# Kernel optimization log

Hardware: AMD Instinct MI355X
Metric: run time of the kernel (lower is better)

Reference implementation:

```python
import jax, jax.numpy as jnp
import numpy as np

D = (96, 96, 96)          # per-item tensor shape (input_shape)
BATCH = 8
R1, R2 = 32, 16           # ranks for the two multi-resolution partitions
MAX_ITER = 15             # fixed ALS iteration count (torch default 100 w/ early stop)


def setup_inputs() -> dict:
    key = jax.random.key(0)
    k = jax.random.split(key, 5)
    m, n = D[0], D[1] * D[2]  # unfold: (first mode, rest) -> (96, 9216)
    return {
        "x": jax.random.normal(k[0], (BATCH,) + D, dtype=jnp.float32),
        "A0_1": jax.random.normal(k[1], (m, R1), dtype=jnp.float32),
        "B0_1": jax.random.normal(k[2], (n, R1), dtype=jnp.float32),
        "A0_2": jax.random.normal(k[3], (m, R2), dtype=jnp.float32),
        "B0_2": jax.random.normal(k[4], (n, R2), dtype=jnp.float32),
    }


def _clean(f):
    # torch.nan_to_num(f, nan=0.0, posinf=1e10, neginf=-1e10)
    return jnp.nan_to_num(f, nan=0.0, posinf=1e10, neginf=-1e10)


def _als(X, A, B):
    """2-mode PARAFAC == ALS matrix factorization. X: (m,n), A: (m,r), B: (n,r)."""
    def step(carry, _):
        A, B = carry
        # mode 0: khatri-rao prod is just B; V = B^T B; A = (X B) pinv(V)
        A = _clean((X @ B) @ jnp.linalg.pinv(B.T @ B))
        # mode 1: unfold is X^T; V = A^T A; B = (X^T A) pinv(V)
        B = _clean((X.T @ A) @ jnp.linalg.pinv(A.T @ A))
        return (A, B), None
    (A, B), _ = jax.lax.scan(step, (A, B), None, length=MAX_ITER)
    return A, B


def _per_item(t, A0_1, B0_1, A0_2, B0_2):
    m = D[0]
    # partition 1 ([[0],[1,2]]): unfold -> (96, 9216)
    X1 = t.reshape(m, -1)
    A1, B1 = _als(X1, A0_1, B0_1)
    approx1 = (A1 @ B1.T).reshape(D)
    residual = t - approx1
    # partition 2 ([[0,1],[2]]): same identity mode order -> same unfold shape
    X2 = residual.reshape(m, -1)
    A2, B2 = _als(X2, A0_2, B0_2)
    approx2 = (A2 @ B2.T).reshape(D)
    # reconstruct() = sum of partition approximations
    return approx1 + approx2


def reference(x, A0_1, B0_1, A0_2, B0_2):
    # per-item MRLR reconstruction, vmapped over the batch (torch loops per item)
    return jax.vmap(_per_item, in_axes=(0, None, None, None, None))(
        x, A0_1, B0_1, A0_2, B0_2
    )
```

## Files before the change

### kernel.cpp

```cpp
#include <hip/hip_runtime.h>


#define TID ((int)threadIdx.x)
typedef float4 f4;

#define SC27 (1.0f/134217728.0f)

__device__ __forceinline__ f4 ld4(const float* p) { return *(const f4*)p; }
__device__ __forceinline__ void st4(float* p, f4 v) { *(f4*)p = v; }
__device__ __forceinline__ f4 f4zero() { return make_float4(0.f,0.f,0.f,0.f); }
__device__ __forceinline__ f4 add4(f4 a, f4 b){ return make_float4(a.x+b.x,a.y+b.y,a.z+b.z,a.w+b.w); }
__device__ __forceinline__ f4 sub4(f4 a, f4 b){ return make_float4(a.x-b.x,a.y-b.y,a.z-b.z,a.w-b.w); }
__device__ __forceinline__ f4 scl4(f4 a, float s){ return make_float4(a.x*s,a.y*s,a.z*s,a.w*s); }
__device__ __forceinline__ void fma4(f4& a, float s, f4 v) {
  a.x = fmaf(s,v.x,a.x); a.y = fmaf(s,v.y,a.y); a.z = fmaf(s,v.z,a.z); a.w = fmaf(s,v.w,a.w);
}
__device__ __forceinline__ float dot4(f4 a, f4 b, float acc) {
  acc = fmaf(a.x,b.x,acc); acc = fmaf(a.y,b.y,acc);
  acc = fmaf(a.z,b.z,acc); acc = fmaf(a.w,b.w,acc); return acc;
}
__device__ __forceinline__ void trimap(int t, int& ti, int& tj) {
  int rem = t; ti = 0;
  #pragma unroll
  for (int r = 0; r < 12; ++r) { int w = 12 - r; if (rem < w) { ti = r; break; } rem -= w; }
  tj = ti + rem;
}
__device__ __forceinline__ void init8(f4 acc[8][2]) {
  #pragma unroll
  for (int a = 0; a < 8; ++a) { acc[a][0] = f4zero(); acc[a][1] = f4zero(); }
}
__device__ __forceinline__ void tile8_step(f4 acc[8][2], const float* u, const float* v) {
  f4 u0 = ld4(u), u1 = ld4(u+4), v0 = ld4(v), v1 = ld4(v+4);
  float aa[8] = {u0.x,u0.y,u0.z,u0.w,u1.x,u1.y,u1.z,u1.w};
  #pragma unroll
  for (int a = 0; a < 8; ++a) { fma4(acc[a][0], aa[a], v0); fma4(acc[a][1], aa[a], v1); }
}

__global__ __launch_bounds__(512) void k1_partials(
    const float* __restrict__ x, const float* __restrict__ b01,
    const float* __restrict__ b02, float* __restrict__ part,
    int nch, int nsc) {
  __shared__ __align__(16) float Xst[48][100];
  __shared__ __align__(16) float Bs[48][52];
  __shared__ __align__(16) float red[9600];
  int bid = blockIdx.x;
  int item = bid & 7, kc = bid >> 3;
  const float* X = x + (size_t)item * 96 * 9216;
  float* base = part + (size_t)(item * nch + kc) * 9600;

  int t = TID, kh = 0, tt = 0;
  const float* ap = nullptr; const float* bp = nullptr;
  float* op = nullptr; int os = 0; bool isM = false;
  bool active = (t < 450);
  if (active) {
    kh = t / 150; tt = t % 150;
    if (tt < 78) {
      int ti, tj; trimap(tt, ti, tj);
      ap = &Xst[0][ti*8]; bp = &Xst[0][tj*8];
      op = base + tt*64; os = 8; isM = true;
    } else {
      int u = tt - 78; int i0 = (u/6)*8, c0 = (u%6)*8;
      ap = &Xst[0][i0]; bp = &Bs[0][c0];
      op = base + 4992 + i0*48 + c0; os = 48;
    }
  }

  f4 acc[8][2]; init8(acc);

  for (int sc = 0; sc < nsc; ++sc) {
    int k0 = (kc * nsc + sc) * 48;
    __syncthreads();
    for (int e = TID; e < 1152; e += 512) {
      int i = e / 12, kq = (e % 12) * 4;
      f4 v = ld4(&X[(size_t)i * 9216 + k0 + kq]);
      Xst[kq][i] = v.x; Xst[kq+1][i] = v.y; Xst[kq+2][i] = v.z; Xst[kq+3][i] = v.w;
    }
    for (int e = TID; e < 384; e += 512) {
      int kk = e / 8, cq = (e % 8) * 4;
      st4(&Bs[kk][cq], ld4(&b01[(size_t)(k0 + kk) * 32 + cq]));
    }
    for (int e = TID; e < 192; e += 512) {
      int kk = e / 4, cq = (e % 4) * 4;
      st4(&Bs[kk][32+cq], ld4(&b02[(size_t)(k0 + kk) * 16 + cq]));
    }
    __syncthreads();
    if (active) {
      int asr = 100, bsr = isM ? 100 : 52;
      const float* ar = ap + kh * asr;
      const float* br = bp + kh * bsr;
      #pragma unroll 4
      for (int kk = kh; kk < 48; kk += 3) {
        tile8_step(acc, ar, br);
        ar += 3 * asr; br += 3 * bsr;
      }
    }
  }
  __syncthreads();
  if (active && kh == 1) {
    #pragma unroll
    for (int a = 0; a < 8; ++a) { st4(&red[tt*64+a*8], acc[a][0]); st4(&red[tt*64+a*8+4], acc[a][1]); }
  }
  __syncthreads();
  if (active && kh == 0) {
    #pragma unroll
    for (int a = 0; a < 8; ++a) {
      acc[a][0] = add4(acc[a][0], ld4(&red[tt*64+a*8]));
      acc[a][1] = add4(acc[a][1], ld4(&red[tt*64+a*8+4]));
    }
  }
  __syncthreads();
  if (active && kh == 2) {
    #pragma unroll
    for (int a = 0; a < 8; ++a) { st4(&red[tt*64+a*8], acc[a][0]); st4(&red[tt*64+a*8+4], acc[a][1]); }
  }
  __syncthreads();
  if (active && kh == 0) {
    #pragma unroll
    for (int a = 0; a < 8; ++a) {
      f4 s0 = add4(acc[a][0], ld4(&red[tt*64+a*8]));
      f4 s1 = add4(acc[a][1], ld4(&red[tt*64+a*8+4]));
      st4(op + a*os, s0); st4(op + a*os + 4, s1);
    }
  }
}

__global__ __launch_bounds__(128) void k2_reduce(
    const float* __restrict__ part, float* __restrict__ Mb,
    float* __restrict__ Cb, int nch) {
  int bid = blockIdx.x;
  int item = bid & 7, chunk = bid >> 3;
  if (TID >= 120) return;
  int q4 = chunk * 120 + TID;
  int off = q4 * 4;
  const float* p = part + (size_t)item * nch * 9600 + off;
  f4 s = f4zero();
  #pragma unroll 8
  for (int c = 0; c < nch; ++c) s = add4(s, ld4(p + (size_t)c * 9600));
  if (off < 4992) {
    int tile = off >> 6, w = (off & 63) >> 2;
    int r = w >> 1, cq = (w & 1) * 4;
    int ti, tj; trimap(tile, ti, tj);
    int i = ti*8 + r, j = tj*8 + cq;
    float* Mi = Mb + (size_t)item * 9216;
    st4(&Mi[i*96 + j], s);
    Mi[(j+0)*96 + i] = s.x; Mi[(j+1)*96 + i] = s.y;
    Mi[(j+2)*96 + i] = s.z; Mi[(j+3)*96 + i] = s.w;
  } else {
    st4(&Cb[(size_t)item * 4608 + (off - 4992)], s);
  }
}

__global__ __launch_bounds__(256) void kw_phase(
    const float* __restrict__ Ag, const float* __restrict__ Bg,
    const float* __restrict__ Subg, float* __restrict__ Dg, float scale,
    const float* __restrict__ Tin, int ti_istr, int tis, int tsub,
    float* __restrict__ Tout, int to_istr, int tos, int TW) {
  __shared__ __align__(16) float Bs[96][100];
  __shared__ __align__(16) float As[8][100];
  __shared__ __align__(16) float Ts[96][36];
  int bid = blockIdx.x;
  int item = bid & 7, w = bid >> 3, t = TID;
  const float* A = Ag + (size_t)item * 9216;

  if (w < 12) {
    const float* B = Bg + (size_t)item * 9216;
    for (int e = t; e < 2304; e += 256) {
      int r = e / 24, cq = (e % 24) * 4;
      st4(&Bs[r][cq], ld4(&B[r*96 + cq]));
    }
    if (t < 192) {
      int r = t / 24, cq = (t % 24) * 4;
      st4(&As[r][cq], ld4(&A[(size_t)(w*8 + r)*96 + cq]));
    }
    __syncthreads();
    if (t < 192) {
      int rl = t / 24, jb = (t % 24) * 4;
      f4 acc = f4zero();
      #pragma unroll 8
      for (int k = 0; k < 96; ++k) fma4(acc, As[rl][k], ld4(&Bs[k][jb]));
      int r = w*8 + rl;
      if (Subg) acc = sub4(ld4(&Subg[(size_t)item*9216 + r*96 + jb]), acc);
      else      acc = scl4(acc, scale);
      st4(&Dg[(size_t)item*9216 + r*96 + jb], acc);
    }
  } else {
    for (int e = t; e < 2304; e += 256) {
      int r = e / 24, cq = (e % 24) * 4;
      st4(&Bs[r][cq], ld4(&A[r*96 + cq]));
    }
    int nq = TW >> 2;
    const float* Ti = Tin + (size_t)item * ti_istr;
    for (int e = t; e < 96*nq; e += 256) {
      int r = e / nq, cq = (e % nq) * 4;
      st4(&Ts[r][cq], ld4(&Ti[(size_t)r * tis + cq]));
    }
    __syncthreads();
    int nact = (TW == 32) ? 192 : 96;
    if (t < nact) {
      int r  = (TW == 32) ? (t >> 1) : t;
      int c0 = (TW == 32) ? (t & 1) * 16 : 0;
      f4 acc[4] = {f4zero(), f4zero(), f4zero(), f4zero()};
      #pragma unroll 4
      for (int k = 0; k < 96; ++k) {
        float a = Bs[r][k];
        const float* tr = &Ts[k][c0];
        fma4(acc[0], a, ld4(tr));   fma4(acc[1], a, ld4(tr+4));
        fma4(acc[2], a, ld4(tr+8)); fma4(acc[3], a, ld4(tr+12));
      }
      if (tsub) {
        #pragma unroll
        for (int u = 0; u < 4; ++u) acc[u] = sub4(ld4(&Ts[r][c0 + u*4]), acc[u]);
      }
      float* To = Tout + (size_t)item * to_istr;
      #pragma unroll
      for (int u = 0; u < 4; ++u) st4(&To[(size_t)r * tos + c0 + u*4], acc[u]);
    }
  }
}

template<int R>
__device__ void gj_wave(float (*aug)[64], int lane) {
  float col[R];
  if (lane < R) {
    #pragma unroll
    for (int i = 0; i < R; ++i) col[i] = aug[i][lane];
  } else {
    #pragma unroll
    for (int i = 0; i < R; ++i) col[i] = (i == lane - R) ? 1.f : 0.f;
  }
  #pragma unroll
  for (int c = 0; c < R; ++c) {
    float pc = __shfl(col[c], c);
    float rp = 1.f / pc;
    bool isc = (lane == c);
    #pragma unroll
    for (int i = 0; i < R; ++i) {
      if (i == c) continue;
      float fi = __shfl(col[i], c) * rp;
      float v = fmaf(-fi, col[c], col[i]);
      col[i] = isc ? 0.f : v;
    }
  }
  #pragma unroll
  for (int i = 0; i < R; ++i) {
    float d = __shfl(col[i], i);
    col[i] = col[i] / d;
  }
  if (lane >= R) {
    #pragma unroll
    for (int i = 0; i < R; ++i) aug[i][lane] = col[i];
  }
}

template<int TW, int MODE>
__global__ __launch_bounds__(256) void kWproj(
    const float* __restrict__ S3g, const float* __restrict__ Pg,
    float* __restrict__ W1g, float* __restrict__ Tgg) {
  __shared__ __align__(16) float S3s[96][100];
  __shared__ __align__(16) float Ps[96][32];
  __shared__ __align__(16) float Qs[96][32];
  __shared__ __align__(16) float aug[32][64];
  __shared__ __align__(16) float QKs[8][32];

  int bid = blockIdx.x;
  int item = bid & 7, w = bid >> 3, t = TID;
  const float* S3 = S3g + (size_t)item * 9216;
  const float* P  = Pg  + (size_t)item * 3072;
  float* W1 = W1g + (size_t)item * 9216;
  float* Tg = Tgg + (size_t)item * 9216;
  const int nq = TW >> 2;

  for (int e = t; e < 2304; e += 256) {
    int r = e / 24, cq = (e % 24) * 4;
    st4(&S3s[r][cq], ld4(&S3[r*96 + cq]));
  }
  for (int e = t; e < 96*nq; e += 256) {
    int r = e / nq, cq = (e % nq) * 4;
    st4(&Ps[r][cq], ld4(&P[r*32 + cq]));
  }
  __syncthreads();

  for (int e = t; e < 96*nq; e += 256) {
    int r = e / nq, c4 = (e % nq) * 4;
    f4 acc = f4zero();
    #pragma unroll 4
    for (int k = 0; k < 96; ++k) fma4(acc, S3s[r][k], ld4(&Ps[k][c4]));
    st4(&Qs[r][c4], acc);
  }
  __syncthreads();

  for (int e = t; e < TW*nq; e += 256) {
    int ar = e / nq, b4 = (e % nq) * 4;
    f4 acc = f4zero();
    #pragma unroll 4
    for (int k = 0; k < 96; ++k) fma4(acc, Qs[k][ar], ld4(&Qs[k][b4]));
    st4(&aug[ar][b4], acc);
  }
  __syncthreads();

  if (t < 2*TW) gj_wave<TW>(aug, t);
  __syncthreads();
  for (int e = t; e < TW*TW; e += 256) { int m = e/TW, c = e%TW; aug[c][m] = aug[m][TW+c]; }
  __syncthreads();

  for (int e = t; e < 8*TW; e += 256) {
    int rr = e / TW, c = e % TW;
    const float* qrow = &Qs[w*8 + rr][0];
    float acc = 0.f;
    #pragma unroll
    for (int m4 = 0; m4 < TW; m4 += 4)
      acc = dot4(ld4(&qrow[m4]), ld4(&aug[c][m4]), acc);
    QKs[rr][c] = acc;
  }
  __syncthreads();

  if (t < 192) {
    int rr = t / 24, jb = (t % 24) * 4;
    int r = w*8 + rr;
    f4 acc = f4zero();
    #pragma unroll
    for (int c4 = 0; c4 < TW; c4 += 4) {
      f4 qk = ld4(&QKs[rr][c4]);
      acc.x = dot4(qk, ld4(&Qs[jb+0][c4]), acc.x);
      acc.y = dot4(qk, ld4(&Qs[jb+1][c4]), acc.y);
      acc.z = dot4(qk, ld4(&Qs[jb+2][c4]), acc.z);
      acc.w = dot4(qk, ld4(&Qs[jb+3][c4]), acc.w);
    }
    if (MODE == 1) st4(&W1[r*96 + jb], acc);
    else           st4(&Tg[r*96 + jb], add4(acc, ld4(&W1[r*96 + jb])));
  }
}

__global__ __launch_bounds__(256) void k4_out(
    const float* __restrict__ x, const float* __restrict__ Tgg,
    float* __restrict__ out) {
  __shared__ __align__(16) float Tt[96][100];
  int bid = blockIdx.x;
  int item = bid & 7, jb = bid >> 3;
  const float* Tg = Tgg + (size_t)item * 9216;
  for (int e = TID * 4; e < 9216; e += 1024) {
    f4 v = ld4(&Tg[e]);
    int i = e / 96, k = e % 96;
    Tt[k][i] = v.x; Tt[k+1][i] = v.y; Tt[k+2][i] = v.z; Tt[k+3][i] = v.w;
  }
  __syncthreads();

  int jq = (TID % 32) * 4, ig = TID / 32;
  int i0 = ig * 12;
  int col = jb * 128 + jq;
  const float* X = x + (size_t)item * 96 * 9216;
  f4 acc[12];
  #pragma unroll
  for (int a = 0; a < 12; ++a) acc[a] = f4zero();

  for (int k = 0; k < 96; ++k) {
    f4 xv = ld4(&X[(size_t)k * 9216 + col]);
    f4 t0 = ld4(&Tt[k][i0]), t1 = ld4(&Tt[k][i0+4]), t2 = ld4(&Tt[k][i0+8]);
    fma4(acc[0], t0.x, xv); fma4(acc[1], t0.y, xv); fma4(acc[2], t0.z, xv); fma4(acc[3], t0.w, xv);
    fma4(acc[4], t1.x, xv); fma4(acc[5], t1.y, xv); fma4(acc[6], t1.z, xv); fma4(acc[7], t1.w, xv);
    fma4(acc[8], t2.x, xv); fma4(acc[9], t2.y, xv); fma4(acc[10], t2.z, xv); fma4(acc[11], t2.w, xv);
  }
  float* O = out + (size_t)item * 96 * 9216;
  #pragma unroll
  for (int a = 0; a < 12; ++a) st4(&O[(size_t)(i0 + a) * 9216 + col], acc[a]);
}

extern "C" void kernel_launch(void* const* d_in, const int* in_sizes, int n_in,
                              void* d_out, int out_size, void* d_ws, size_t ws_size,
                              hipStream_t stream) {
  (void)in_sizes; (void)n_in; (void)out_size;
  const float* x   = (const float*)d_in[0];
  const float* b01 = (const float*)d_in[2];
  const float* b02 = (const float*)d_in[4];
  float* out = (float*)d_out;
  float* ws  = (float*)d_ws;

  const size_t EXTRA = 73728ull*6 + 36864 + 24576*2 + 12288;
  int nch = (ws_size >= ((size_t)64*8*9600 + EXTRA) * sizeof(float)) ? 64 : 32;
  int nsc = 9216 / nch / 48;

  float* Mb  = ws + (size_t)nch * 8 * 9600;
  float* Cb  = Mb  + 73728;
  float* Sb  = Cb  + 36864;
  float* S2b = Sb  + 73728;
  float* S3b = S2b + 73728;
  float* W1b = S3b + 73728;
  float* Tgb = W1b + 73728;
  float* Pb  = Tgb + 73728;
  float* Yb  = Pb  + 24576;
  float* CPb = Yb  + 24576;

  k1_partials<<<dim3(nch*8), 512, 0, stream>>>(x, b01, b02, ws, nch, nsc);
  k2_reduce<<<dim3(160), 128, 0, stream>>>(ws, Mb, Cb, nch);

  kw_phase<<<dim3(96),256,0,stream>>>(Mb, Mb, nullptr, Sb, SC27,
      nullptr,0,0,0, nullptr,0,0, 0);
  kw_phase<<<dim3(104),256,0,stream>>>(Sb, Sb, nullptr, S2b, 1.f,
      Cb,4608,48,0, Yb,3072,32, 32);
  kw_phase<<<dim3(104),256,0,stream>>>(S2b, S2b, nullptr, S3b, 1.f,
      Yb,3072,32,0, Pb,3072,32, 32);
  kWproj<32,1><<<dim3(96),256,0,stream>>>(S3b, Pb, W1b, Tgb);

  kw_phase<<<dim3(104),256,0,stream>>>(W1b, Mb, Mb, Sb, 1.f,
      Cb+32,4608,48,1, CPb,1536,16, 16);
  kw_phase<<<dim3(96),256,0,stream>>>(Sb, W1b, Sb, Mb, 1.f,
      nullptr,0,0,0, nullptr,0,0, 0);

  kw_phase<<<dim3(96),256,0,stream>>>(Mb, Mb, nullptr, Sb, SC27,
      nullptr,0,0,0, nullptr,0,0, 0);
  kw_phase<<<dim3(104),256,0,stream>>>(Sb, Sb, nullptr, S2b, 1.f,
      CPb,1536,16,0, Yb,3072,32, 16);
  kw_phase<<<dim3(104),256,0,stream>>>(S2b, S2b, nullptr, S3b, 1.f,
      Yb,3072,32,0, Pb,3072,32, 16);
  kWproj<16,2><<<dim3(96),256,0,stream>>>(S3b, Pb, W1b, Tgb);

  k4_out<<<dim3(576), 256, 0, stream>>>(x, Tgb, out);
}
```

Measured before the change: 181.4 us.

## Fuse reduce and small-matrix phases into one persistent kernel with grid barriers

Replaces the k2_reduce launch and the chain of kw_phase and kWproj launches with one cooperative kernel of 104 workgroups. The workgroups synchronise through an atomic grid barrier held in workspace and zeroed by a memset before each run. This removes about a dozen kernel launch gaps on a small latency-bound workload. The S3 product is also restructured into thin slab products (S2·(S2·Y)), so the full 96x96 S3 matrix is no longer formed. The change relies on all 104 workgroups being resident at the same time, and the spin barrier could deadlock if they are not.

```diff
diff --git a/kernel.cpp b/kernel.cpp
--- a/kernel.cpp
+++ b/kernel.cpp
@@ -5,6 +5,7 @@
 typedef float4 f4;
 
 #define SC27 (1.0f/134217728.0f)
+#define NWG  104
 
 __device__ __forceinline__ f4 ld4(const float* p) { return *(const f4*)p; }
 __device__ __forceinline__ void st4(float* p, f4 v) { *(f4*)p = v; }
@@ -34,6 +35,24 @@
   float aa[8] = {u0.x,u0.y,u0.z,u0.w,u1.x,u1.y,u1.z,u1.w};
   #pragma unroll
   for (int a = 0; a < 8; ++a) { fma4(acc[a][0], aa[a], v0); fma4(acc[a][1], aa[a], v1); }
+}
+
+__device__ __forceinline__ void gridbar(unsigned* bar, unsigned nwg) {
+  __syncthreads();
+  if (threadIdx.x == 0) {
+    __threadfence();
+    unsigned g = __hip_atomic_load(bar + 1, __ATOMIC_RELAXED, __HIP_MEMORY_SCOPE_AGENT);
+    unsigned a = __hip_atomic_fetch_add(bar, 1u, __ATOMIC_ACQ_REL, __HIP_MEMORY_SCOPE_AGENT);
+    if (a == nwg - 1u) {
+      __hip_atomic_store(bar, 0u, __ATOMIC_RELAXED, __HIP_MEMORY_SCOPE_AGENT);
+      __hip_atomic_store(bar + 1, g + 1u, __ATOMIC_RELEASE, __HIP_MEMORY_SCOPE_AGENT);
+    } else {
+      while (__hip_atomic_load(bar + 1, __ATOMIC_ACQUIRE, __HIP_MEMORY_SCOPE_AGENT) == g)
+        __builtin_amdgcn_s_sleep(8);
+    }
+    __threadfence();
+  }
+  __syncthreads();
 }
 
 __global__ __launch_bounds__(512) void k1_partials(
@@ -124,106 +143,12 @@
   }
 }
 
-__global__ __launch_bounds__(128) void k2_reduce(
-    const float* __restrict__ part, float* __restrict__ Mb,
-    float* __restrict__ Cb, int nch) {
-  int bid = blockIdx.x;
-  int item = bid & 7, chunk = bid >> 3;
-  if (TID >= 120) return;
-  int q4 = chunk * 120 + TID;
-  int off = q4 * 4;
-  const float* p = part + (size_t)item * nch * 9600 + off;
-  f4 s = f4zero();
-  #pragma unroll 8
-  for (int c = 0; c < nch; ++c) s = add4(s, ld4(p + (size_t)c * 9600));
-  if (off < 4992) {
-    int tile = off >> 6, w = (off & 63) >> 2;
-    int r = w >> 1, cq = (w & 1) * 4;
-    int ti, tj; trimap(tile, ti, tj);
-    int i = ti*8 + r, j = tj*8 + cq;
-    float* Mi = Mb + (size_t)item * 9216;
-    st4(&Mi[i*96 + j], s);
-    Mi[(j+0)*96 + i] = s.x; Mi[(j+1)*96 + i] = s.y;
-    Mi[(j+2)*96 + i] = s.z; Mi[(j+3)*96 + i] = s.w;
-  } else {
-    st4(&Cb[(size_t)item * 4608 + (off - 4992)], s);
-  }
-}
-
-__global__ __launch_bounds__(256) void kw_phase(
-    const float* __restrict__ Ag, const float* __restrict__ Bg,
-    const float* __restrict__ Subg, float* __restrict__ Dg, float scale,
-    const float* __restrict__ Tin, int ti_istr, int tis, int tsub,
-    float* __restrict__ Tout, int to_istr, int tos, int TW) {
-  __shared__ __align__(16) float Bs[96][100];
-  __shared__ __align__(16) float As[8][100];
-  __shared__ __align__(16) float Ts[96][36];
-  int bid = blockIdx.x;
-  int item = bid & 7, w = bid >> 3, t = TID;
-  const float* A = Ag + (size_t)item * 9216;
-
-  if (w < 12) {
-    const float* B = Bg + (size_t)item * 9216;
-    for (int e = t; e < 2304; e += 256) {
-      int r = e / 24, cq = (e % 24) * 4;
-      st4(&Bs[r][cq], ld4(&B[r*96 + cq]));
-    }
-    if (t < 192) {
-      int r = t / 24, cq = (t % 24) * 4;
-      st4(&As[r][cq], ld4(&A[(size_t)(w*8 + r)*96 + cq]));
-    }
-    __syncthreads();
-    if (t < 192) {
-      int rl = t / 24, jb = (t % 24) * 4;
-      f4 acc = f4zero();
-      #pragma unroll 8
-      for (int k = 0; k < 96; ++k) fma4(acc, As[rl][k], ld4(&Bs[k][jb]));
-      int r = w*8 + rl;
-      if (Subg) acc = sub4(ld4(&Subg[(size_t)item*9216 + r*96 + jb]), acc);
-      else      acc = scl4(acc, scale);
-      st4(&Dg[(size_t)item*9216 + r*96 + jb], acc);
-    }
-  } else {
-    for (int e = t; e < 2304; e += 256) {
-      int r = e / 24, cq = (e % 24) * 4;
-      st4(&Bs[r][cq], ld4(&A[r*96 + cq]));
-    }
-    int nq = TW >> 2;
-    const float* Ti = Tin + (size_t)item * ti_istr;
-    for (int e = t; e < 96*nq; e += 256) {
-      int r = e / nq, cq = (e % nq) * 4;
-      st4(&Ts[r][cq], ld4(&Ti[(size_t)r * tis + cq]));
-    }
-    __syncthreads();
-    int nact = (TW == 32) ? 192 : 96;
-    if (t < nact) {
-      int r  = (TW == 32) ? (t >> 1) : t;
-      int c0 = (TW == 32) ? (t & 1) * 16 : 0;
-      f4 acc[4] = {f4zero(), f4zero(), f4zero(), f4zero()};
-      #pragma unroll 4
-      for (int k = 0; k < 96; ++k) {
-        float a = Bs[r][k];
-        const float* tr = &Ts[k][c0];
-        fma4(acc[0], a, ld4(tr));   fma4(acc[1], a, ld4(tr+4));
-        fma4(acc[2], a, ld4(tr+8)); fma4(acc[3], a, ld4(tr+12));
-      }
-      if (tsub) {
-        #pragma unroll
-        for (int u = 0; u < 4; ++u) acc[u] = sub4(ld4(&Ts[r][c0 + u*4]), acc[u]);
-      }
-      float* To = Tout + (size_t)item * to_istr;
-      #pragma unroll
-      for (int u = 0; u < 4; ++u) st4(&To[(size_t)r * tos + c0 + u*4], acc[u]);
-    }
-  }
-}
-
 template<int R>
-__device__ void gj_wave(float (*aug)[64], int lane) {
+__device__ void gj_wave(float* aug, int lane) {
   float col[R];
   if (lane < R) {
     #pragma unroll
-    for (int i = 0; i < R; ++i) col[i] = aug[i][lane];
+    for (int i = 0; i < R; ++i) col[i] = aug[i*68 + lane];
   } else {
     #pragma unroll
     for (int i = 0; i < R; ++i) col[i] = (i == lane - R) ? 1.f : 0.f;
@@ -248,86 +173,271 @@
   }
   if (lane >= R) {
     #pragma unroll
-    for (int i = 0; i < R; ++i) aug[i][lane] = col[i];
-  }
-}
-
-template<int TW, int MODE>
-__global__ __launch_bounds__(256) void kWproj(
-    const float* __restrict__ S3g, const float* __restrict__ Pg,
-    float* __restrict__ W1g, float* __restrict__ Tgg) {
-  __shared__ __align__(16) float S3s[96][100];
-  __shared__ __align__(16) float Ps[96][32];
-  __shared__ __align__(16) float Qs[96][32];
-  __shared__ __align__(16) float aug[32][64];
-  __shared__ __align__(16) float QKs[8][32];
-
-  int bid = blockIdx.x;
-  int item = bid & 7, w = bid >> 3, t = TID;
-  const float* S3 = S3g + (size_t)item * 9216;
-  const float* P  = Pg  + (size_t)item * 3072;
-  float* W1 = W1g + (size_t)item * 9216;
-  float* Tg = Tgg + (size_t)item * 9216;
-  const int nq = TW >> 2;
-
+    for (int i = 0; i < R; ++i) aug[i*68 + lane] = col[i];
+  }
+}
+
+__device__ __forceinline__ void stage_full(float* Bs, const float* src, int t) {
   for (int e = t; e < 2304; e += 256) {
     int r = e / 24, cq = (e % 24) * 4;
-    st4(&S3s[r][cq], ld4(&S3[r*96 + cq]));
-  }
+    st4(&Bs[r*100 + cq], ld4(&src[r*96 + cq]));
+  }
+}
+__device__ __forceinline__ void stage_slab(float* As, const float* src, int row0, int t) {
+  if (t < 192) {
+    int r = t / 24, cq = (t % 24) * 4;
+    st4(&As[r*100 + cq], ld4(&src[(size_t)(row0 + r)*96 + cq]));
+  }
+}
+__device__ __forceinline__ void stage_thin(float* Ts, const float* src, int istr, int nq, int t) {
   for (int e = t; e < 96*nq; e += 256) {
     int r = e / nq, cq = (e % nq) * 4;
-    st4(&Ps[r][cq], ld4(&P[r*32 + cq]));
-  }
-  __syncthreads();
-
+    st4(&Ts[r*36 + cq], ld4(&src[(size_t)r*istr + cq]));
+  }
+}
+__device__ __forceinline__ void square_slab(const float* As, const float* Bs,
+    const float* Sub, float* D, float scale, int w, int t) {
+  if (t < 192) {
+    int rl = t / 24, jb = (t % 24) * 4;
+    f4 acc = f4zero();
+    #pragma unroll 8
+    for (int k = 0; k < 96; ++k) fma4(acc, As[rl*100 + k], ld4(&Bs[k*100 + jb]));
+    int r = w*8 + rl;
+    if (Sub) acc = sub4(ld4(&Sub[r*96 + jb]), acc);
+    else     acc = scl4(acc, scale);
+    st4(&D[r*96 + jb], acc);
+  }
+}
+__device__ __forceinline__ void thin_full(const float* A100, const float* Ts,
+    float* To, int tos, int TW, int tsub, int t) {
+  int nact = (TW == 32) ? 192 : 96;
+  if (t < nact) {
+    int r  = (TW == 32) ? (t >> 1) : t;
+    int c0 = (TW == 32) ? (t & 1) * 16 : 0;
+    f4 acc[4] = {f4zero(), f4zero(), f4zero(), f4zero()};
+    #pragma unroll 4
+    for (int k = 0; k < 96; ++k) {
+      float a = A100[r*100 + k];
+      const float* tr = &Ts[k*36 + c0];
+      fma4(acc[0], a, ld4(tr));   fma4(acc[1], a, ld4(tr+4));
+      fma4(acc[2], a, ld4(tr+8)); fma4(acc[3], a, ld4(tr+12));
+    }
+    if (tsub) {
+      #pragma unroll
+      for (int u = 0; u < 4; ++u) acc[u] = sub4(ld4(&Ts[r*36 + c0 + u*4]), acc[u]);
+    }
+    #pragma unroll
+    for (int u = 0; u < 4; ++u) st4(&To[(size_t)r*tos + c0 + u*4], acc[u]);
+  }
+}
+__device__ __forceinline__ void thin_slab(const float* As, const float* Ts,
+    float* To, int w, int TW, int t) {
+  int nq = TW >> 2;
+  if (t < 8*nq) {
+    int rl = t / nq, c4 = (t % nq) * 4;
+    f4 acc = f4zero();
+    #pragma unroll 8
+    for (int k = 0; k < 96; ++k) fma4(acc, As[rl*100 + k], ld4(&Ts[k*36 + c4]));
+    st4(&To[(size_t)(w*8 + rl)*32 + c4], acc);
+  }
+}
+
+template<int TW>
+__device__ void proj_phase(const float* Bs , float* Ps, float* Qs,
+    float* aug, float* QKs, const float* Pg, float* Wdst, const float* Wadd,
+    int w, int t) {
+  const int nq = TW >> 2;
+  stage_thin(Ps, Pg, 32, nq, t);
+  __syncthreads();
   for (int e = t; e < 96*nq; e += 256) {
     int r = e / nq, c4 = (e % nq) * 4;
     f4 acc = f4zero();
     #pragma unroll 4
-    for (int k = 0; k < 96; ++k) fma4(acc, S3s[r][k], ld4(&Ps[k][c4]));
-    st4(&Qs[r][c4], acc);
-  }
-  __syncthreads();
-
+    for (int k = 0; k < 96; ++k) fma4(acc, Bs[r*100 + k], ld4(&Ps[k*36 + c4]));
+    st4(&Qs[r*36 + c4], acc);
+  }
+  __syncthreads();
   for (int e = t; e < TW*nq; e += 256) {
     int ar = e / nq, b4 = (e % nq) * 4;
     f4 acc = f4zero();
     #pragma unroll 4
-    for (int k = 0; k < 96; ++k) fma4(acc, Qs[k][ar], ld4(&Qs[k][b4]));
-    st4(&aug[ar][b4], acc);
-  }
-  __syncthreads();
-
+    for (int k = 0; k < 96; ++k) fma4(acc, Qs[k*36 + ar], ld4(&Qs[k*36 + b4]));
+    st4(&aug[ar*68 + b4], acc);
+  }
+  __syncthreads();
   if (t < 2*TW) gj_wave<TW>(aug, t);
   __syncthreads();
-  for (int e = t; e < TW*TW; e += 256) { int m = e/TW, c = e%TW; aug[c][m] = aug[m][TW+c]; }
-  __syncthreads();
-
+  for (int e = t; e < TW*TW; e += 256) {
+    int m = e / TW, c = e % TW;
+    aug[c*68 + m] = aug[m*68 + TW + c];
+  }
+  __syncthreads();
   for (int e = t; e < 8*TW; e += 256) {
     int rr = e / TW, c = e % TW;
-    const float* qrow = &Qs[w*8 + rr][0];
     float acc = 0.f;
     #pragma unroll
     for (int m4 = 0; m4 < TW; m4 += 4)
-      acc = dot4(ld4(&qrow[m4]), ld4(&aug[c][m4]), acc);
-    QKs[rr][c] = acc;
-  }
-  __syncthreads();
-
+      acc = dot4(ld4(&Qs[(w*8 + rr)*36 + m4]), ld4(&aug[c*68 + m4]), acc);
+    QKs[rr*32 + c] = acc;
+  }
+  __syncthreads();
   if (t < 192) {
     int rr = t / 24, jb = (t % 24) * 4;
     int r = w*8 + rr;
     f4 acc = f4zero();
     #pragma unroll
     for (int c4 = 0; c4 < TW; c4 += 4) {
-      f4 qk = ld4(&QKs[rr][c4]);
-      acc.x = dot4(qk, ld4(&Qs[jb+0][c4]), acc.x);
-      acc.y = dot4(qk, ld4(&Qs[jb+1][c4]), acc.y);
-      acc.z = dot4(qk, ld4(&Qs[jb+2][c4]), acc.z);
-      acc.w = dot4(qk, ld4(&Qs[jb+3][c4]), acc.w);
-    }
-    if (MODE == 1) st4(&W1[r*96 + jb], acc);
-    else           st4(&Tg[r*96 + jb], add4(acc, ld4(&W1[r*96 + jb])));
+      f4 qk = ld4(&QKs[rr*32 + c4]);
+      acc.x = dot4(qk, ld4(&Qs[(jb+0)*36 + c4]), acc.x);
+      acc.y = dot4(qk, ld4(&Qs[(jb+1)*36 + c4]), acc.y);
+      acc.z = dot4(qk, ld4(&Qs[(jb+2)*36 + c4]), acc.z);
+      acc.w = dot4(qk, ld4(&Qs[(jb+3)*36 + c4]), acc.w);
+    }
+    if (Wadd) acc = add4(acc, ld4(&Wadd[r*96 + jb]));
+    st4(&Wdst[r*96 + jb], acc);
+  }
+}
+
+__global__ __launch_bounds__(256) void kcoop(
+    float* __restrict__ part, float* __restrict__ Mb, float* __restrict__ Cb,
+    float* __restrict__ Sb, float* __restrict__ S2b, float* __restrict__ W1b,
+    float* __restrict__ Tgb, float* __restrict__ Yb, float* __restrict__ Pb,
+    float* __restrict__ CPb, unsigned* __restrict__ bar, int nch) {
+  __shared__ __align__(16) float smem[18944];
+  float* Bs  = smem;
+  float* As  = smem + 9600;
+  float* Ts  = smem + 10400;
+  float* Ps  = smem + 9600;
+  float* Qs  = smem + 13056;
+  float* aug = smem + 16512;
+  float* QKs = smem + 18688;
+
+  int wg = blockIdx.x, t = TID;
+  int item = wg & 7, w = wg >> 3;
+  float* Mi  = Mb  + (size_t)item * 9216;
+  float* Ci  = Cb  + (size_t)item * 4608;
+  float* S1i = Sb  + (size_t)item * 9216;
+  float* S2i = S2b + (size_t)item * 9216;
+  float* W1i = W1b + (size_t)item * 9216;
+  float* Tgi = Tgb + (size_t)item * 9216;
+  float* Yi  = Yb  + (size_t)item * 3072;
+  float* Pi  = Pb  + (size_t)item * 3072;
+  float* CPi = CPb + (size_t)item * 1536;
+
+  {
+    int q4 = w * 185 + t;
+    if (t < 185 && q4 < 2400) {
+      int off = q4 * 4;
+      const float* p = part + (size_t)item * nch * 9600 + off;
+      f4 s = f4zero();
+      #pragma unroll 8
+      for (int c = 0; c < nch; ++c) s = add4(s, ld4(p + (size_t)c * 9600));
+      if (off < 4992) {
+        int tile = off >> 6, ww = (off & 63) >> 2;
+        int r = ww >> 1, cq = (ww & 1) * 4;
+        int ti, tj; trimap(tile, ti, tj);
+        int i = ti*8 + r, j = tj*8 + cq;
+        st4(&Mi[i*96 + j], s);
+        Mi[(j+0)*96 + i] = s.x; Mi[(j+1)*96 + i] = s.y;
+        Mi[(j+2)*96 + i] = s.z; Mi[(j+3)*96 + i] = s.w;
+      } else {
+        st4(&Ci[off - 4992], s);
+      }
+    }
+  }
+  gridbar(bar, NWG);
+
+  if (w < 12) {
+    stage_full(Bs, Mi, t); stage_slab(As, Mi, w*8, t);
+    __syncthreads();
+    square_slab(As, Bs, nullptr, S1i, SC27, w, t);
+  }
+  gridbar(bar, NWG);
+
+  if (w < 12) {
+    stage_full(Bs, S1i, t); stage_slab(As, S1i, w*8, t);
+    __syncthreads();
+    square_slab(As, Bs, nullptr, S2i, 1.f, w, t);
+  } else {
+    stage_full(Bs, S1i, t); stage_thin(Ts, Ci, 48, 8, t);
+    __syncthreads();
+    thin_full(Bs, Ts, Yi, 32, 32, 0, t);
+  }
+  gridbar(bar, NWG);
+
+  if (w < 12) {
+    stage_slab(As, S2i, w*8, t); stage_thin(Ts, Yi, 32, 8, t);
+    __syncthreads();
+    thin_slab(As, Ts, Pi, w, 32, t);
+  }
+  gridbar(bar, NWG);
+
+  if (w < 12) {
+    stage_slab(As, S2i, w*8, t); stage_thin(Ts, Pi, 32, 8, t);
+    __syncthreads();
+    thin_slab(As, Ts, Yi, w, 32, t);
+  }
+  gridbar(bar, NWG);
+
+  if (w < 12) {
+    stage_full(Bs, S2i, t);
+    proj_phase<32>(Bs, Ps, Qs, aug, QKs, Yi, W1i, nullptr, w, t);
+  }
+  gridbar(bar, NWG);
+
+  if (w < 12) {
+    stage_full(Bs, Mi, t); stage_slab(As, W1i, w*8, t);
+    __syncthreads();
+    square_slab(As, Bs, Mi, S1i, 1.f, w, t);
+  } else {
+    stage_full(Bs, W1i, t); stage_thin(Ts, Ci + 32, 48, 4, t);
+    __syncthreads();
+    thin_full(Bs, Ts, CPi, 16, 16, 1, t);
+  }
+  gridbar(bar, NWG);
+
+  if (w < 12) {
+    stage_full(Bs, W1i, t); stage_slab(As, S1i, w*8, t);
+    __syncthreads();
+    square_slab(As, Bs, S1i, Mi, 1.f, w, t);
+  }
+  gridbar(bar, NWG);
+
+  if (w < 12) {
+    stage_full(Bs, Mi, t); stage_slab(As, Mi, w*8, t);
+    __syncthreads();
+    square_slab(As, Bs, nullptr, S1i, SC27, w, t);
+  }
+  gridbar(bar, NWG);
+
+  if (w < 12) {
+    stage_full(Bs, S1i, t); stage_slab(As, S1i, w*8, t);
+    __syncthreads();
+    square_slab(As, Bs, nullptr, S2i, 1.f, w, t);
+  } else {
+    stage_full(Bs, S1i, t); stage_thin(Ts, CPi, 16, 4, t);
+    __syncthreads();
+    thin_full(Bs, Ts, Yi, 32, 16, 0, t);
+  }
+  gridbar(bar, NWG);
+
+  if (w < 12) {
+    stage_slab(As, S2i, w*8, t); stage_thin(Ts, Yi, 32, 4, t);
+    __syncthreads();
+    thin_slab(As, Ts, Pi, w, 16, t);
+  }
+  gridbar(bar, NWG);
+
+  if (w < 12) {
+    stage_slab(As, S2i, w*8, t); stage_thin(Ts, Pi, 32, 4, t);
+    __syncthreads();
+    thin_slab(As, Ts, Yi, w, 16, t);
+  }
+  gridbar(bar, NWG);
+
+  if (w < 12) {
+    stage_full(Bs, S2i, t);
+    proj_phase<16>(Bs, Ps, Qs, aug, QKs, Yi, Tgi, W1i, w, t);
   }
 }
 
@@ -375,7 +485,7 @@
   float* out = (float*)d_out;
   float* ws  = (float*)d_ws;
 
-  const size_t EXTRA = 73728ull*6 + 36864 + 24576*2 + 12288;
+  const size_t EXTRA = 73728ull*5 + 36864 + 24576*2 + 12288 + 16;
   int nch = (ws_size >= ((size_t)64*8*9600 + EXTRA) * sizeof(float)) ? 64 : 32;
   int nsc = 9216 / nch / 48;
 
@@ -383,36 +493,16 @@
   float* Cb  = Mb  + 73728;
   float* Sb  = Cb  + 36864;
   float* S2b = Sb  + 73728;
-  float* S3b = S2b + 73728;
-  float* W1b = S3b + 73728;
+  float* W1b = S2b + 73728;
   float* Tgb = W1b + 73728;
-  float* Pb  = Tgb + 73728;
-  float* Yb  = Pb  + 24576;
-  float* CPb = Yb  + 24576;
-
+  float* Yb  = Tgb + 73728;
+  float* Pb  = Yb  + 24576;
+  float* CPb = Pb  + 24576;
+  unsigned* bar = (unsigned*)(CPb + 12288);
+
+  hipMemsetAsync((void*)bar, 0, 16, stream);
   k1_partials<<<dim3(nch*8), 512, 0, stream>>>(x, b01, b02, ws, nch, nsc);
-  k2_reduce<<<dim3(160), 128, 0, stream>>>(ws, Mb, Cb, nch);
-
-  kw_phase<<<dim3(96),256,0,stream>>>(Mb, Mb, nullptr, Sb, SC27,
-      nullptr,0,0,0, nullptr,0,0, 0);
-  kw_phase<<<dim3(104),256,0,stream>>>(Sb, Sb, nullptr, S2b, 1.f,
-      Cb,4608,48,0, Yb,3072,32, 32);
-  kw_phase<<<dim3(104),256,0,stream>>>(S2b, S2b, nullptr, S3b, 1.f,
-      Yb,3072,32,0, Pb,3072,32, 32);
-  kWproj<32,1><<<dim3(96),256,0,stream>>>(S3b, Pb, W1b, Tgb);
-
-  kw_phase<<<dim3(104),256,0,stream>>>(W1b, Mb, Mb, Sb, 1.f,
-      Cb+32,4608,48,1, CPb,1536,16, 16);
-  kw_phase<<<dim3(96),256,0,stream>>>(Sb, W1b, Sb, Mb, 1.f,
-      nullptr,0,0,0, nullptr,0,0, 0);
-
-  kw_phase<<<dim3(96),256,0,stream>>>(Mb, Mb, nullptr, Sb, SC27,
-      nullptr,0,0,0, nullptr,0,0, 0);
-  kw_phase<<<dim3(104),256,0,stream>>>(Sb, Sb, nullptr, S2b, 1.f,
-      CPb,1536,16,0, Yb,3072,32, 16);
-  kw_phase<<<dim3(104),256,0,stream>>>(S2b, S2b, nullptr, S3b, 1.f,
-      Yb,3072,32,0, Pb,3072,32, 16);
-  kWproj<16,2><<<dim3(96),256,0,stream>>>(S3b, Pb, W1b, Tgb);
-
+  kcoop<<<dim3(NWG), 256, 0, stream>>>(ws, Mb, Cb, Sb, S2b, W1b, Tgb,
+                                       Yb, Pb, CPb, bar, nch);
   k4_out<<<dim3(576), 256, 0, stream>>>(x, Tgb, out);
 }
```

Result: slower. 281.9 us (+55.4%).

## Fuse final squaring phase into projection kernel via repeated local multiplies

Applied to the files above, without the earlier changes.

Removes the separate kw_phase launch that computed S3 = S2·S2 and P = S2·Y. Instead, kWproj3 loads S2 once into shared memory and applies it three times to Y (ping-ponging between two shared buffers) to get Q = S2^3·Y directly. Shared-memory arrays are flattened with padded strides. This cuts one launch and the associated global round-trip per partition, but each block now redundantly performs three 96x96xTW products.

```diff
diff --git a/kernel.cpp b/kernel.cpp
--- a/kernel.cpp
+++ b/kernel.cpp
@@ -219,11 +219,11 @@
 }
 
 template<int R>
-__device__ void gj_wave(float (*aug)[64], int lane) {
+__device__ void gj_wave(float* aug, int lane) {
   float col[R];
   if (lane < R) {
     #pragma unroll
-    for (int i = 0; i < R; ++i) col[i] = aug[i][lane];
+    for (int i = 0; i < R; ++i) col[i] = aug[i*68 + lane];
   } else {
     #pragma unroll
     for (int i = 0; i < R; ++i) col[i] = (i == lane - R) ? 1.f : 0.f;
@@ -248,69 +248,77 @@
   }
   if (lane >= R) {
     #pragma unroll
-    for (int i = 0; i < R; ++i) aug[i][lane] = col[i];
+    for (int i = 0; i < R; ++i) aug[i*68 + lane] = col[i];
   }
 }
 
 template<int TW, int MODE>
-__global__ __launch_bounds__(256) void kWproj(
-    const float* __restrict__ S3g, const float* __restrict__ Pg,
+__global__ __launch_bounds__(256) void kWproj3(
+    const float* __restrict__ Sg, const float* __restrict__ Yg,
     float* __restrict__ W1g, float* __restrict__ Tgg) {
-  __shared__ __align__(16) float S3s[96][100];
-  __shared__ __align__(16) float Ps[96][32];
-  __shared__ __align__(16) float Qs[96][32];
-  __shared__ __align__(16) float aug[32][64];
-  __shared__ __align__(16) float QKs[8][32];
+  __shared__ __align__(16) float smem[18944];
+  float* Bs  = smem;
+  float* Ta  = smem + 9600;
+  float* Tb  = smem + 13056;
+  float* aug = smem + 16512;
+  float* QKs = smem + 18688;
 
   int bid = blockIdx.x;
   int item = bid & 7, w = bid >> 3, t = TID;
-  const float* S3 = S3g + (size_t)item * 9216;
-  const float* P  = Pg  + (size_t)item * 3072;
+  const float* S = Sg + (size_t)item * 9216;
+  const float* Y = Yg + (size_t)item * 3072;
   float* W1 = W1g + (size_t)item * 9216;
   float* Tg = Tgg + (size_t)item * 9216;
   const int nq = TW >> 2;
 
   for (int e = t; e < 2304; e += 256) {
     int r = e / 24, cq = (e % 24) * 4;
-    st4(&S3s[r][cq], ld4(&S3[r*96 + cq]));
+    st4(&Bs[r*100 + cq], ld4(&S[r*96 + cq]));
   }
   for (int e = t; e < 96*nq; e += 256) {
     int r = e / nq, cq = (e % nq) * 4;
-    st4(&Ps[r][cq], ld4(&P[r*32 + cq]));
-  }
-  __syncthreads();
-
-  for (int e = t; e < 96*nq; e += 256) {
-    int r = e / nq, c4 = (e % nq) * 4;
-    f4 acc = f4zero();
-    #pragma unroll 4
-    for (int k = 0; k < 96; ++k) fma4(acc, S3s[r][k], ld4(&Ps[k][c4]));
-    st4(&Qs[r][c4], acc);
-  }
-  __syncthreads();
+    st4(&Ta[r*36 + cq], ld4(&Y[r*32 + cq]));
+  }
+  __syncthreads();
+
+  #pragma unroll
+  for (int pass = 0; pass < 3; ++pass) {
+    const float* src = (pass & 1) ? Tb : Ta;
+    float* dst       = (pass & 1) ? Ta : Tb;
+    for (int e = t; e < 96*nq; e += 256) {
+      int r = e / nq, c4 = (e % nq) * 4;
+      f4 acc = f4zero();
+      #pragma unroll 4
+      for (int k = 0; k < 96; ++k) fma4(acc, Bs[r*100 + k], ld4(&src[k*36 + c4]));
+      st4(&dst[r*36 + c4], acc);
+    }
+    __syncthreads();
+  }
 
   for (int e = t; e < TW*nq; e += 256) {
     int ar = e / nq, b4 = (e % nq) * 4;
     f4 acc = f4zero();
     #pragma unroll 4
-    for (int k = 0; k < 96; ++k) fma4(acc, Qs[k][ar], ld4(&Qs[k][b4]));
-    st4(&aug[ar][b4], acc);
+    for (int k = 0; k < 96; ++k) fma4(acc, Tb[k*36 + ar], ld4(&Tb[k*36 + b4]));
+    st4(&aug[ar*68 + b4], acc);
   }
   __syncthreads();
 
   if (t < 2*TW) gj_wave<TW>(aug, t);
   __syncthreads();
-  for (int e = t; e < TW*TW; e += 256) { int m = e/TW, c = e%TW; aug[c][m] = aug[m][TW+c]; }
+  for (int e = t; e < TW*TW; e += 256) {
+    int m = e / TW, c = e % TW;
+    aug[c*68 + m] = aug[m*68 + TW + c];
+  }
   __syncthreads();
 
   for (int e = t; e < 8*TW; e += 256) {
     int rr = e / TW, c = e % TW;
-    const float* qrow = &Qs[w*8 + rr][0];
     float acc = 0.f;
     #pragma unroll
     for (int m4 = 0; m4 < TW; m4 += 4)
-      acc = dot4(ld4(&qrow[m4]), ld4(&aug[c][m4]), acc);
-    QKs[rr][c] = acc;
+      acc = dot4(ld4(&Tb[(w*8 + rr)*36 + m4]), ld4(&aug[c*68 + m4]), acc);
+    QKs[rr*32 + c] = acc;
   }
   __syncthreads();
 
@@ -320,11 +328,11 @@
     f4 acc = f4zero();
     #pragma unroll
     for (int c4 = 0; c4 < TW; c4 += 4) {
-      f4 qk = ld4(&QKs[rr][c4]);
-      acc.x = dot4(qk, ld4(&Qs[jb+0][c4]), acc.x);
-      acc.y = dot4(qk, ld4(&Qs[jb+1][c4]), acc.y);
-      acc.z = dot4(qk, ld4(&Qs[jb+2][c4]), acc.z);
-      acc.w = dot4(qk, ld4(&Qs[jb+3][c4]), acc.w);
+      f4 qk = ld4(&QKs[rr*32 + c4]);
+      acc.x = dot4(qk, ld4(&Tb[(jb+0)*36 + c4]), acc.x);
+      acc.y = dot4(qk, ld4(&Tb[(jb+1)*36 + c4]), acc.y);
+      acc.z = dot4(qk, ld4(&Tb[(jb+2)*36 + c4]), acc.z);
+      acc.w = dot4(qk, ld4(&Tb[(jb+3)*36 + c4]), acc.w);
     }
     if (MODE == 1) st4(&W1[r*96 + jb], acc);
     else           st4(&Tg[r*96 + jb], add4(acc, ld4(&W1[r*96 + jb])));
@@ -375,7 +383,7 @@
   float* out = (float*)d_out;
   float* ws  = (float*)d_ws;
 
-  const size_t EXTRA = 73728ull*6 + 36864 + 24576*2 + 12288;
+  const size_t EXTRA = 73728ull*5 + 36864 + 24576 + 12288;
   int nch = (ws_size >= ((size_t)64*8*9600 + EXTRA) * sizeof(float)) ? 64 : 32;
   int nsc = 9216 / nch / 48;
 
@@ -383,11 +391,9 @@
   float* Cb  = Mb  + 73728;
   float* Sb  = Cb  + 36864;
   float* S2b = Sb  + 73728;
-  float* S3b = S2b + 73728;
-  float* W1b = S3b + 73728;
+  float* W1b = S2b + 73728;
   float* Tgb = W1b + 73728;
-  float* Pb  = Tgb + 73728;
-  float* Yb  = Pb  + 24576;
+  float* Yb  = Tgb + 73728;
   float* CPb = Yb  + 24576;
 
   k1_partials<<<dim3(nch*8), 512, 0, stream>>>(x, b01, b02, ws, nch, nsc);
@@ -397,9 +403,7 @@
       nullptr,0,0,0, nullptr,0,0, 0);
   kw_phase<<<dim3(104),256,0,stream>>>(Sb, Sb, nullptr, S2b, 1.f,
       Cb,4608,48,0, Yb,3072,32, 32);
-  kw_phase<<<dim3(104),256,0,stream>>>(S2b, S2b, nullptr, S3b, 1.f,
-      Yb,3072,32,0, Pb,3072,32, 32);
-  kWproj<32,1><<<dim3(96),256,0,stream>>>(S3b, Pb, W1b, Tgb);
+  kWproj3<32,1><<<dim3(96),256,0,stream>>>(S2b, Yb, W1b, Tgb);
 
   kw_phase<<<dim3(104),256,0,stream>>>(W1b, Mb, Mb, Sb, 1.f,
       Cb+32,4608,48,1, CPb,1536,16, 16);
@@ -410,9 +414,7 @@
       nullptr,0,0,0, nullptr,0,0, 0);
   kw_phase<<<dim3(104),256,0,stream>>>(Sb, Sb, nullptr, S2b, 1.f,
       CPb,1536,16,0, Yb,3072,32, 16);
-  kw_phase<<<dim3(104),256,0,stream>>>(S2b, S2b, nullptr, S3b, 1.f,
-      Yb,3072,32,0, Pb,3072,32, 16);
-  kWproj<16,2><<<dim3(96),256,0,stream>>>(S3b, Pb, W1b, Tgb);
+  kWproj3<16,2><<<dim3(96),256,0,stream>>>(S2b, Yb, W1b, Tgb);
 
   k4_out<<<dim3(576), 256, 0, stream>>>(x, Tgb, out);
 }
```

New measurement: 177.9 us. Within noise of the previous version (-1.9%).
